# Optimization experiments

Measured on AMD Instinct MI355X. Metric: run time of the kernel, lower is better.

## Reference

```python
import jax, jax.numpy as jnp
import numpy as np

HEADS = 16
LN_EPS = 1e-5

def setup_inputs() -> dict:
    key = jax.random.key(0)
    ks = jax.random.split(key, 8)
    B, S, NT = 4, 1024, 1024
    sc = 1.0 / np.sqrt(NT)
    return {
        "x": jax.random.normal(ks[0], (B, S, NT), dtype=jnp.float32),
        "Wq": jax.random.normal(ks[1], (NT, NT), dtype=jnp.float32) * sc,
        "bq": jax.random.normal(ks[2], (NT,), dtype=jnp.float32) * 0.02,
        "Wk": jax.random.normal(ks[3], (NT, NT), dtype=jnp.float32) * sc,
        "bk": jax.random.normal(ks[4], (NT,), dtype=jnp.float32) * 0.02,
        "Wv": jax.random.normal(ks[5], (NT, NT), dtype=jnp.float32) * sc,
        "bv": jax.random.normal(ks[6], (NT,), dtype=jnp.float32) * 0.02,
        "gamma": jnp.ones((NT,), dtype=jnp.float32),
        "beta": jnp.zeros((NT,), dtype=jnp.float32),
    }

def reference(x, Wq, bq, Wk, bk, Wv, bv, gamma, beta):
    B, S, nt = x.shape
    heads = HEADS
    dph = nt // heads
    # torch nn.Linear: y = x @ W.T + b
    q = x @ Wq.T + bq
    k = x @ Wk.T + bk
    v = x @ Wv.T + bv
    # torch .view(B*heads, -1, dph) is a row-major reshape (interleaved split)
    q = q.reshape(B * heads, -1, dph)
    k = k.reshape(B * heads, -1, dph)
    v = v.reshape(B * heads, -1, dph)
    # scaled scores; scale uses last dim of the score matrix (== seq len here)
    att = jnp.einsum('bid,bjd->bij', q, k)
    scale = att.shape[-1] ** (-0.5)
    att = jax.nn.softmax(jax.nn.relu(att * scale), axis=-1)
    # dropout in eval mode -> identity
    at_sum_sum = att.sum(axis=1).reshape(B, heads, -1)  # [B, heads, S]
    context = jnp.einsum('bij,bjd->bid', att, v).reshape(B, -1, nt)
    h = x + context
    mu = h.mean(axis=-1, keepdims=True)
    var = h.var(axis=-1, keepdims=True)
    out = (h - mu) * jax.lax.rsqrt(var + LN_EPS) * gamma + beta
    return out, at_sum_sum
```

## Files before the change

### kernel.cpp

```cpp
#include <hip/hip_runtime.h>
#include <hip/hip_bf16.h>
#include <cstdint>
#include <cstddef>


typedef short short8 __attribute__((ext_vector_type(8)));
typedef short short4v __attribute__((ext_vector_type(4)));
typedef float f32x4 __attribute__((ext_vector_type(4)));

#define MFMA32(a, b, c) __builtin_amdgcn_mfma_f32_16x16x32_bf16(a, b, c, 0, 0, 0)
#define MFMA16x16(a, b, c) __builtin_amdgcn_mfma_f32_16x16x16bf16_1k(a, b, c, 0, 0, 0)
#define QSCALE 0.045084220027780106f

__device__ __forceinline__ short f2bf(float f) {
  union { float f; uint32_t u; } x; x.f = f;
  uint32_t u = x.u + 0x7fffu + ((x.u >> 16) & 1u);
  return (short)(u >> 16);
}

__device__ __forceinline__ uint32_t pk_bf16_trunc(float lo, float hi) {
  return __builtin_amdgcn_perm(__float_as_uint(hi), __float_as_uint(lo),
                               0x07060302u);
}

#define GLDS16(gp, lp)                                                        \
  __builtin_amdgcn_global_load_lds(                                           \
      (const __attribute__((address_space(1))) void*)(gp),                    \
      (__attribute__((address_space(3))) void*)(lp), 16, 0, 0)

__global__ __launch_bounds__(256) void convert_kernel(
    const float* __restrict__ x, const float* __restrict__ wq,
    const float* __restrict__ wk, const float* __restrict__ wv,
    short* __restrict__ xb, short* __restrict__ wb,
    float* __restrict__ out2) {
  if (blockIdx.x >= 7168) {
    const int idx = (blockIdx.x - 7168) * 256 + threadIdx.x;
    *(f32x4*)(out2 + (size_t)idx * 4) = (f32x4){0.f, 0.f, 0.f, 0.f};
    return;
  }
  const long XN = 4L * 1024 * 1024, WN = 1024L * 1024;
  long e = (long)(blockIdx.x * blockDim.x + threadIdx.x) * 4;
  const float* src; short* dst;
  if (e < XN)               { src = x  + e;                dst = xb + e; }
  else if (e < XN + WN)     { src = wq + (e - XN);         dst = wb + (e - XN); }
  else if (e < XN + 2 * WN) { src = wk + (e - XN - WN);    dst = wb + (e - XN); }
  else                      { src = wv + (e - XN - 2*WN);  dst = wb + (e - XN); }
  f32x4 v = *(const f32x4*)src;
  short4v o;
  o[0] = f2bf(v[0]); o[1] = f2bf(v[1]); o[2] = f2bf(v[2]); o[3] = f2bf(v[3]);
  *(short4v*)dst = o;
}

__global__ __launch_bounds__(256, 3) void qkv_gemm(
    const short* __restrict__ xb, const short* __restrict__ wb,
    const float* __restrict__ bq, const float* __restrict__ bk,
    const float* __restrict__ bv, short* __restrict__ qb,
    short* __restrict__ kb, short* __restrict__ vtp) {
  __shared__ short As[128 * 64];
  __shared__ short Bs[128 * 64];
  const int tid = threadIdx.x;
  const int lane = tid & 63;
  const int lm = lane & 15, quad = lane >> 4;
  const int wave = tid >> 6, wy = wave >> 1, wx = wave & 1;
  const int f = blockIdx.x + (blockIdx.y << 3);
  const int r8 = f & 7, s = f >> 3;
  const int m0 = (((r8 >> 1) << 3) + (s & 7)) * 128;
  const int n0 = (((r8 & 1) << 2) + (s >> 3)) * 128;
  const int z = blockIdx.z;
  const short* w = wb + (size_t)z * (1024 * 1024);
  const float* bias = (z == 0) ? bq : (z == 1) ? bk : bv;
  const float scl = (z == 0) ? QSCALE : 1.0f;

  const int srow = tid >> 3;
  const int schk = (tid & 7) ^ (srow & 7);
  const short* gA = xb + (size_t)(m0 + srow) * 1024 + schk * 8;
  const short* gB = w  + (size_t)(n0 + srow) * 1024 + schk * 8;
  short* lA = As + tid * 8;
  short* lB = Bs + tid * 8;

  f32x4 acc[4][4];
#pragma unroll
  for (int i = 0; i < 4; i++)
#pragma unroll
    for (int j = 0; j < 4; j++) acc[i][j] = (f32x4){0.f, 0.f, 0.f, 0.f};

  for (int k0 = 0; k0 < 1024; k0 += 64) {
#pragma unroll
    for (int q = 0; q < 4; q++) {
      GLDS16(gA + k0 + q * 32 * 1024, lA + q * 2048);
      GLDS16(gB + k0 + q * 32 * 1024, lB + q * 2048);
    }
    __syncthreads();
#pragma unroll
    for (int ks = 0; ks < 2; ks++) {
      const int ck = (((ks << 2) + quad) ^ (lm & 7)) * 8;
      short8 a[4], b[4];
#pragma unroll
      for (int t = 0; t < 4; t++) {
        a[t] = *(const short8*)(As + (wy * 64 + t * 16 + lm) * 64 + ck);
        b[t] = *(const short8*)(Bs + (wx * 64 + t * 16 + lm) * 64 + ck);
      }
#pragma unroll
      for (int mt = 0; mt < 4; mt++)
#pragma unroll
        for (int nt = 0; nt < 4; nt++)
          acc[mt][nt] = MFMA32(a[mt], b[nt], acc[mt][nt]);
    }
    __syncthreads();
  }
  if (z == 2) {
#pragma unroll
    for (int nt = 0; nt < 4; nt++) {
      const int n = n0 + wx * 64 + nt * 16 + lm;
      const float bn = bias[n];
      const size_t nbase = (size_t)((n >> 4) & 3) * 16384 +
                           (size_t)((((n >> 8) & 3) * 16 + (n & 15)) * 4 +
                                    ((n >> 6) & 3));
#pragma unroll
      for (int mt = 0; mt < 4; mt++) {
#pragma unroll
        for (int r = 0; r < 4; r++) {
          const int m = m0 + wy * 64 + mt * 16 + quad * 4 + r;
          vtp[(size_t)(m >> 6) * 65536 + nbase + (size_t)(m & 63) * 256] =
              f2bf(acc[mt][nt][r] + bn);
        }
      }
    }
  } else {
    short* out = (z == 0) ? qb : kb;
#pragma unroll
    for (int nt = 0; nt < 4; nt++) {
      const int n = n0 + wx * 64 + nt * 16 + lm;
      const float bn = bias[n];
#pragma unroll
      for (int mt = 0; mt < 4; mt++) {
        const int mb = m0 + wy * 64 + mt * 16 + quad * 4;
#pragma unroll
        for (int r = 0; r < 4; r++)
          out[(size_t)(mb + r) * 1024 + n] = f2bf((acc[mt][nt][r] + bn) * scl);
      }
    }
  }
}

__global__ __launch_bounds__(256, 2) void attn_kernel(
    const short* __restrict__ qb, const short* __restrict__ kb,
    const short* __restrict__ vtp, const float* __restrict__ x,
    const float* __restrict__ gamma, const float* __restrict__ beta,
    float* __restrict__ out1, float* __restrict__ rvW) {
  __shared__ short Ks[3][64 * 64];

  const int tid = threadIdx.x;
  const int lane = tid & 63, wave = tid >> 6;
  const int lm = lane & 15, quad = lane >> 4;
  const int bid = blockIdx.x;
  const int h = ((bid >> 6) << 3) + (bid & 7);
  const int bb = (bid >> 3) & 7;
  const short* Qh = qb + (size_t)h * 65536;
  const short* Kh = kb + (size_t)h * 65536;
  const short* Vp = vtp + (size_t)h * 65536;
  const int i0 = bb * 128 + wave * 32;

  const short8 qA0 = *(const short8*)(Qh + (size_t)(i0 + lm) * 64 + quad * 8);
  const short8 qA1 = *(const short8*)(Qh + (size_t)(i0 + lm) * 64 + 32 + quad * 8);
  const short8 qB0 = *(const short8*)(Qh + (size_t)(i0 + 16 + lm) * 64 + quad * 8);
  const short8 qB1 = *(const short8*)(Qh + (size_t)(i0 + 16 + lm) * 64 + 32 + quad * 8);

  const int c0 = tid, c1 = tid + 256;
  const short* gK0 = Kh + (size_t)(c0 >> 3) * 64 + ((c0 & 7) ^ ((c0 >> 3) & 7)) * 8;
  const short* gK1 = Kh + (size_t)(c1 >> 3) * 64 + ((c1 & 7) ^ ((c1 >> 3) & 7)) * 8;
  const int lK0 = c0 * 8, lK1 = c1 * 8;
  const short* vl = Vp + lane * 4;

#define ATTN_STAGE(c, buf)                                                    \
  do {                                                                        \
    const int ko_ = ((c) & 15) * 4096;                                        \
    GLDS16(gK0 + ko_, &Ks[buf][0] + lK0);                                     \
    GLDS16(gK1 + ko_, &Ks[buf][0] + lK1);                                     \
  } while (0)

  f32x4 accA[4], accB[4];
#pragma unroll
  for (int t = 0; t < 4; t++) {
    accA[t] = (f32x4){0.f, 0.f, 0.f, 0.f};
    accB[t] = (f32x4){0.f, 0.f, 0.f, 0.f};
  }
  float dsA[4] = {0.f, 0.f, 0.f, 0.f};
  float dsB[4] = {0.f, 0.f, 0.f, 0.f};

  const int swz0 = (quad ^ (lm & 7)) * 8;
  const int swz1 = ((quad + 4) ^ (lm & 7)) * 8;

  ATTN_STAGE(0, 0);
  ATTN_STAGE(1, 1);

  for (int ch = 0; ch < 16; ch++) {
    const int b = ch % 3, bs = (ch + 2) % 3;
    asm volatile("s_waitcnt vmcnt(2)" ::: "memory");
    __builtin_amdgcn_s_barrier();
    __builtin_amdgcn_s_setprio(1);
    const short* vc = vl + ch * 1024;
#pragma unroll
    for (int jj = 0; jj < 4; jj++) {
      const short* krow = &Ks[b][(jj * 16 + lm) * 64];
      const short8 kf0 = *(const short8*)(krow + swz0);
      const short8 kf1 = *(const short8*)(krow + swz1);
      f32x4 zA = {0.f, 0.f, 0.f, 0.f};
      zA = MFMA32(kf0, qA0, zA);
      zA = MFMA32(kf1, qA1, zA);
      f32x4 zB = {0.f, 0.f, 0.f, 0.f};
      zB = MFMA32(kf0, qB0, zB);
      zB = MFMA32(kf1, qB1, zB);
      float pA[4], pB[4];
#pragma unroll
      for (int r = 0; r < 4; r++) {
        pA[r] = __builtin_amdgcn_exp2f(fmaxf(zA[r], 0.f));
        dsA[r] += pA[r];
        pB[r] = __builtin_amdgcn_exp2f(fmaxf(zB[r], 0.f));
        dsB[r] += pB[r];
      }
      union { uint32_t u[2]; short4v s; } puA, puB;
      puA.u[0] = pk_bf16_trunc(pA[0], pA[1]);
      puA.u[1] = pk_bf16_trunc(pA[2], pA[3]);
      puB.u[0] = pk_bf16_trunc(pB[0], pB[1]);
      puB.u[1] = pk_bf16_trunc(pB[2], pB[3]);
      const short* vj = vc + jj * 256;
#pragma unroll
      for (int dt = 0; dt < 4; dt++) {
        const short4v vtf = *(const short4v*)(vj + dt * 16384);
        accA[dt] = MFMA16x16(vtf, puA.s, accA[dt]);
        accB[dt] = MFMA16x16(vtf, puB.s, accB[dt]);
      }
    }
    __builtin_amdgcn_s_setprio(0);
    if (ch < 15) ATTN_STAGE(ch + 2, bs);
  }
  asm volatile("s_waitcnt vmcnt(0)" ::: "memory");

  float tA = (dsA[0] + dsA[1]) + (dsA[2] + dsA[3]);
  tA += __shfl_xor(tA, 16);
  tA += __shfl_xor(tA, 32);
  float tB = (dsB[0] + dsB[1]) + (dsB[2] + dsB[3]);
  tB += __shfl_xor(tB, 16);
  tB += __shfl_xor(tB, 32);
  const float rvA = 1.f / tA;
  const float rvB = 1.f / tB;
  if (lane < 16) {
    rvW[h * 1024 + i0 + lm] = rvA;
    rvW[h * 1024 + i0 + 16 + lm] = rvB;
  }

  const int mA = h * 64 + bb * 8 + wave * 2;
  const int nb = lm * 64 + quad * 4;
#pragma unroll
  for (int tile = 0; tile < 2; tile++) {
    const int m = mA + tile;
    const f32x4* accT = tile ? accB : accA;
    const float rv = tile ? rvB : rvA;
    const float* xr = x + (size_t)m * 1024;
    float hv[4][4], s1 = 0.f, s2 = 0.f;
#pragma unroll
    for (int dt = 0; dt < 4; dt++) {
      f32x4 xv = *(const f32x4*)(xr + nb + dt * 16);
#pragma unroll
      for (int r = 0; r < 4; r++) {
        const float v = xv[r] + accT[dt][r] * rv;
        hv[dt][r] = v; s1 += v; s2 += v * v;
      }
    }
#pragma unroll
    for (int mk = 1; mk < 64; mk <<= 1) {
      s1 += __shfl_xor(s1, mk);
      s2 += __shfl_xor(s2, mk);
    }
    const float mu = s1 * (1.f / 1024.f);
    const float var = s2 * (1.f / 1024.f) - mu * mu;
    const float rstd = rsqrtf(var + 1e-5f);
    float* orow = out1 + (size_t)m * 1024;
#pragma unroll
    for (int dt = 0; dt < 4; dt++) {
      f32x4 gv = *(const f32x4*)(gamma + nb + dt * 16);
      f32x4 bv2 = *(const f32x4*)(beta + nb + dt * 16);
      f32x4 ov;
#pragma unroll
      for (int r = 0; r < 4; r++)
        ov[r] = (hv[dt][r] - mu) * rstd * gv[r] + bv2[r];
      *(f32x4*)(orow + nb + dt * 16) = ov;
    }
  }
}

__global__ __launch_bounds__(256, 4) void colsum_kernel(
    const short* __restrict__ qb, const short* __restrict__ kb,
    const float* __restrict__ rvW, float* __restrict__ out2) {
  const int tid = threadIdx.x;
  const int lane = tid & 63, wave = tid >> 6;
  const int lm = lane & 15, quad = lane >> 4;
  const int bid = blockIdx.x;
  const int h = ((bid >> 7) << 3) + (bid & 7);
  const int jb = (bid >> 3) & 7;
  const int ih = (bid >> 6) & 1;
  const int j0 = jb * 128 + wave * 32;
  const short* Qh = qb + (size_t)h * 65536 + (size_t)ih * 32768;
  const short* Kh = kb + (size_t)h * 65536;
  const float* rvh = rvW + h * 1024 + ih * 512;

  const short* krA = Kh + (size_t)(j0 + lm) * 64 + quad * 8;
  const short8 kA0 = *(const short8*)krA;
  const short8 kA1 = *(const short8*)(krA + 32);
  const short* krB = Kh + (size_t)(j0 + 16 + lm) * 64 + quad * 8;
  const short8 kB0 = *(const short8*)krB;
  const short8 kB1 = *(const short8*)(krB + 32);

  f32x4 csA = {0.f, 0.f, 0.f, 0.f};
  f32x4 csB = {0.f, 0.f, 0.f, 0.f};

  for (int ch = 0; ch < 8; ch++) {
    const short* qc = Qh + ch * 4096 + (size_t)lm * 64 + quad * 8;
    const float* rvc = rvh + ch * 64 + lm;
    __builtin_amdgcn_s_setprio(1);
#pragma unroll
    for (int ii = 0; ii < 4; ii++) {
      const short* qrow = qc + ii * 1024;
      const short8 qf0 = *(const short8*)qrow;
      const short8 qf1 = *(const short8*)(qrow + 32);
      f32x4 zA = {0.f, 0.f, 0.f, 0.f};
      zA = MFMA32(kA0, qf0, zA);
      zA = MFMA32(kA1, qf1, zA);
      f32x4 zB = {0.f, 0.f, 0.f, 0.f};
      zB = MFMA32(kB0, qf0, zB);
      zB = MFMA32(kB1, qf1, zB);
      const float rvv = rvc[ii * 16];
#pragma unroll
      for (int r = 0; r < 4; r++) {
        csA[r] += __builtin_amdgcn_exp2f(fmaxf(zA[r], 0.f)) * rvv;
        csB[r] += __builtin_amdgcn_exp2f(fmaxf(zB[r], 0.f)) * rvv;
      }
    }
    __builtin_amdgcn_s_setprio(0);
  }

#pragma unroll
  for (int mk = 1; mk < 16; mk <<= 1)
#pragma unroll
    for (int r = 0; r < 4; r++) {
      csA[r] += __shfl_xor(csA[r], mk);
      csB[r] += __shfl_xor(csB[r], mk);
    }
  if (lm == 0) {
    float* pA = out2 + h * 1024 + j0 + quad * 4;
    float* pB = pA + 16;
#pragma unroll
    for (int r = 0; r < 4; r++) {
      atomicAdd(pA + r, csA[r]);
      atomicAdd(pB + r, csB[r]);
    }
  }
}

extern "C" void kernel_launch(void* const* d_in, const int* in_sizes, int n_in,
                              void* d_out, int out_size, void* d_ws, size_t ws_size,
                              hipStream_t stream) {
  const float* x  = (const float*)d_in[0];
  const float* Wq = (const float*)d_in[1];
  const float* bq = (const float*)d_in[2];
  const float* Wk = (const float*)d_in[3];
  const float* bk = (const float*)d_in[4];
  const float* Wv = (const float*)d_in[5];
  const float* bv = (const float*)d_in[6];
  const float* gamma = (const float*)d_in[7];
  const float* beta  = (const float*)d_in[8];

  float* out1 = (float*)d_out;
  float* out2 = out1 + 4L * 1024 * 1024;

  short* xb = (short*)d_ws;
  short* wb = xb + 4L * 1024 * 1024;
  short* qb = wb + 3L * 1024 * 1024;
  short* kb = qb + 4L * 1024 * 1024;
  short* vtp = kb + 4L * 1024 * 1024;
  float* rvW = (float*)wb;

  convert_kernel<<<7232, 256, 0, stream>>>(x, Wq, Wk, Wv, xb, wb, out2);
  qkv_gemm<<<dim3(8, 32, 3), 256, 0, stream>>>(xb, wb, bq, bk, bv, qb, kb, vtp);
  attn_kernel<<<512, 256, 0, stream>>>(qb, kb, vtp, x, gamma, beta, out1, rvW);
  colsum_kernel<<<1024, 256, 0, stream>>>(qb, kb, rvW, out2);
}
```

Measured before the change: 181.3 us.

## Fuse column-sum pass into attention kernel and stage V through LDS

Removes the separate colsum kernel. After the softmax denominators are known, the attention block recomputes its 128-row slice of scores against all keys, reduces the normalised probabilities per column in LDS, and issues one atomicAdd per column per block. V tiles are now loaded into a triple-buffered shared buffer alongside K, and the prefetch is issued right after the barrier instead of at the end of the loop. This drops a kernel launch and the rvW round trip through global memory. The cost is a second QK pass inside the attention kernel, extra LDS use that may lower occupancy, and more atomics on out2.

```diff
diff --git a/kernel.cpp b/kernel.cpp
--- a/kernel.cpp
+++ b/kernel.cpp
@@ -147,8 +147,9 @@
     const short* __restrict__ qb, const short* __restrict__ kb,
     const short* __restrict__ vtp, const float* __restrict__ x,
     const float* __restrict__ gamma, const float* __restrict__ beta,
-    float* __restrict__ out1, float* __restrict__ rvW) {
+    float* __restrict__ out1, float* __restrict__ out2) {
   __shared__ short Ks[3][64 * 64];
+  __shared__ short Vs[3][4 * 4 * 256];
 
   const int tid = threadIdx.x;
   const int lane = tid & 63, wave = tid >> 6;
@@ -169,10 +170,20 @@
   const int c0 = tid, c1 = tid + 256;
   const short* gK0 = Kh + (size_t)(c0 >> 3) * 64 + ((c0 & 7) ^ ((c0 >> 3) & 7)) * 8;
   const short* gK1 = Kh + (size_t)(c1 >> 3) * 64 + ((c1 & 7) ^ ((c1 >> 3) & 7)) * 8;
+  const short* gV0 = Vp + (c0 >> 7) * 16384 + ((c0 >> 5) & 3) * 256 + (c0 & 31) * 8;
+  const short* gV1 = Vp + (c1 >> 7) * 16384 + ((c1 >> 5) & 3) * 256 + (c1 & 31) * 8;
   const int lK0 = c0 * 8, lK1 = c1 * 8;
-  const short* vl = Vp + lane * 4;
 
 #define ATTN_STAGE(c, buf)                                                    \
+  do {                                                                        \
+    const int ko_ = ((c) & 15) * 4096, vo_ = ((c) & 15) * 1024;               \
+    GLDS16(gK0 + ko_, &Ks[buf][0] + lK0);                                     \
+    GLDS16(gK1 + ko_, &Ks[buf][0] + lK1);                                     \
+    GLDS16(gV0 + vo_, &Vs[buf][0] + lK0);                                     \
+    GLDS16(gV1 + vo_, &Vs[buf][0] + lK1);                                     \
+  } while (0)
+
+#define ATTN_STAGE2(c, buf)                                                   \
   do {                                                                        \
     const int ko_ = ((c) & 15) * 4096;                                        \
     GLDS16(gK0 + ko_, &Ks[buf][0] + lK0);                                     \
@@ -196,10 +207,10 @@
 
   for (int ch = 0; ch < 16; ch++) {
     const int b = ch % 3, bs = (ch + 2) % 3;
-    asm volatile("s_waitcnt vmcnt(2)" ::: "memory");
+    asm volatile("s_waitcnt vmcnt(4)" ::: "memory");
     __builtin_amdgcn_s_barrier();
+    if (ch < 15) ATTN_STAGE(ch + 2, bs);
     __builtin_amdgcn_s_setprio(1);
-    const short* vc = vl + ch * 1024;
 #pragma unroll
     for (int jj = 0; jj < 4; jj++) {
       const short* krow = &Ks[b][(jj * 16 + lm) * 64];
@@ -224,16 +235,15 @@
       puA.u[1] = pk_bf16_trunc(pA[2], pA[3]);
       puB.u[0] = pk_bf16_trunc(pB[0], pB[1]);
       puB.u[1] = pk_bf16_trunc(pB[2], pB[3]);
-      const short* vj = vc + jj * 256;
+      const short* vbase = &Vs[b][jj * 256 + lane * 4];
 #pragma unroll
       for (int dt = 0; dt < 4; dt++) {
-        const short4v vtf = *(const short4v*)(vj + dt * 16384);
+        const short4v vtf = *(const short4v*)(vbase + dt * 1024);
         accA[dt] = MFMA16x16(vtf, puA.s, accA[dt]);
         accB[dt] = MFMA16x16(vtf, puB.s, accB[dt]);
       }
     }
     __builtin_amdgcn_s_setprio(0);
-    if (ch < 15) ATTN_STAGE(ch + 2, bs);
   }
   asm volatile("s_waitcnt vmcnt(0)" ::: "memory");
 
@@ -245,9 +255,56 @@
   tB += __shfl_xor(tB, 32);
   const float rvA = 1.f / tA;
   const float rvB = 1.f / tB;
-  if (lane < 16) {
-    rvW[h * 1024 + i0 + lm] = rvA;
-    rvW[h * 1024 + i0 + 16 + lm] = rvB;
+
+  float rvsA[4], rvsB[4];
+#pragma unroll
+  for (int r = 0; r < 4; r++) {
+    rvsA[r] = __shfl(rvA, quad * 4 + r);
+    rvsB[r] = __shfl(rvB, quad * 4 + r);
+  }
+  __syncthreads();
+  float* cs = (float*)&Vs[0][0];
+
+  ATTN_STAGE2(0, 0);
+  ATTN_STAGE2(1, 1);
+
+  for (int ch = 0; ch < 16; ch++) {
+    const int b = ch % 3, bs = (ch + 2) % 3;
+    asm volatile("s_waitcnt vmcnt(2)" ::: "memory");
+    __builtin_amdgcn_s_barrier();
+    if (ch < 15) ATTN_STAGE2(ch + 2, bs);
+    __builtin_amdgcn_s_setprio(1);
+#pragma unroll
+    for (int jj = 0; jj < 4; jj++) {
+      const short* krow = &Ks[b][(jj * 16 + lm) * 64];
+      const short8 kf0 = *(const short8*)(krow + swz0);
+      const short8 kf1 = *(const short8*)(krow + swz1);
+      f32x4 zA = {0.f, 0.f, 0.f, 0.f};
+      zA = MFMA32(qA0, kf0, zA);
+      zA = MFMA32(qA1, kf1, zA);
+      f32x4 zB = {0.f, 0.f, 0.f, 0.f};
+      zB = MFMA32(qB0, kf0, zB);
+      zB = MFMA32(qB1, kf1, zB);
+      float v = 0.f;
+#pragma unroll
+      for (int r = 0; r < 4; r++) {
+        v += __builtin_amdgcn_exp2f(fmaxf(zA[r], 0.f)) * rvsA[r]
+           + __builtin_amdgcn_exp2f(fmaxf(zB[r], 0.f)) * rvsB[r];
+      }
+      v += __shfl_xor(v, 16);
+      v += __shfl_xor(v, 32);
+      if (quad == 0)
+        cs[wave * 1024 + ch * 64 + jj * 16 + lm] = v;
+    }
+    __builtin_amdgcn_s_setprio(0);
+  }
+  asm volatile("s_waitcnt vmcnt(0)" ::: "memory");
+  __syncthreads();
+#pragma unroll
+  for (int s = 0; s < 4; s++) {
+    const int j = s * 256 + tid;
+    const float t4 = (cs[j] + cs[1024 + j]) + (cs[2048 + j] + cs[3072 + j]);
+    atomicAdd(out2 + h * 1024 + j, t4);
   }
 
   const int mA = h * 64 + bb * 8 + wave * 2;
@@ -286,74 +343,6 @@
       for (int r = 0; r < 4; r++)
         ov[r] = (hv[dt][r] - mu) * rstd * gv[r] + bv2[r];
       *(f32x4*)(orow + nb + dt * 16) = ov;
-    }
-  }
-}
-
-__global__ __launch_bounds__(256, 4) void colsum_kernel(
-    const short* __restrict__ qb, const short* __restrict__ kb,
-    const float* __restrict__ rvW, float* __restrict__ out2) {
-  const int tid = threadIdx.x;
-  const int lane = tid & 63, wave = tid >> 6;
-  const int lm = lane & 15, quad = lane >> 4;
-  const int bid = blockIdx.x;
-  const int h = ((bid >> 7) << 3) + (bid & 7);
-  const int jb = (bid >> 3) & 7;
-  const int ih = (bid >> 6) & 1;
-  const int j0 = jb * 128 + wave * 32;
-  const short* Qh = qb + (size_t)h * 65536 + (size_t)ih * 32768;
-  const short* Kh = kb + (size_t)h * 65536;
-  const float* rvh = rvW + h * 1024 + ih * 512;
-
-  const short* krA = Kh + (size_t)(j0 + lm) * 64 + quad * 8;
-  const short8 kA0 = *(const short8*)krA;
-  const short8 kA1 = *(const short8*)(krA + 32);
-  const short* krB = Kh + (size_t)(j0 + 16 + lm) * 64 + quad * 8;
-  const short8 kB0 = *(const short8*)krB;
-  const short8 kB1 = *(const short8*)(krB + 32);
-
-  f32x4 csA = {0.f, 0.f, 0.f, 0.f};
-  f32x4 csB = {0.f, 0.f, 0.f, 0.f};
-
-  for (int ch = 0; ch < 8; ch++) {
-    const short* qc = Qh + ch * 4096 + (size_t)lm * 64 + quad * 8;
-    const float* rvc = rvh + ch * 64 + lm;
-    __builtin_amdgcn_s_setprio(1);
-#pragma unroll
-    for (int ii = 0; ii < 4; ii++) {
-      const short* qrow = qc + ii * 1024;
-      const short8 qf0 = *(const short8*)qrow;
-      const short8 qf1 = *(const short8*)(qrow + 32);
-      f32x4 zA = {0.f, 0.f, 0.f, 0.f};
-      zA = MFMA32(kA0, qf0, zA);
-      zA = MFMA32(kA1, qf1, zA);
-      f32x4 zB = {0.f, 0.f, 0.f, 0.f};
-      zB = MFMA32(kB0, qf0, zB);
-      zB = MFMA32(kB1, qf1, zB);
-      const float rvv = rvc[ii * 16];
-#pragma unroll
-      for (int r = 0; r < 4; r++) {
-        csA[r] += __builtin_amdgcn_exp2f(fmaxf(zA[r], 0.f)) * rvv;
-        csB[r] += __builtin_amdgcn_exp2f(fmaxf(zB[r], 0.f)) * rvv;
-      }
-    }
-    __builtin_amdgcn_s_setprio(0);
-  }
-
-#pragma unroll
-  for (int mk = 1; mk < 16; mk <<= 1)
-#pragma unroll
-    for (int r = 0; r < 4; r++) {
-      csA[r] += __shfl_xor(csA[r], mk);
-      csB[r] += __shfl_xor(csB[r], mk);
-    }
-  if (lm == 0) {
-    float* pA = out2 + h * 1024 + j0 + quad * 4;
-    float* pB = pA + 16;
-#pragma unroll
-    for (int r = 0; r < 4; r++) {
-      atomicAdd(pA + r, csA[r]);
-      atomicAdd(pB + r, csB[r]);
     }
   }
 }
@@ -379,10 +368,8 @@
   short* qb = wb + 3L * 1024 * 1024;
   short* kb = qb + 4L * 1024 * 1024;
   short* vtp = kb + 4L * 1024 * 1024;
-  float* rvW = (float*)wb;
 
   convert_kernel<<<7232, 256, 0, stream>>>(x, Wq, Wk, Wv, xb, wb, out2);
   qkv_gemm<<<dim3(8, 32, 3), 256, 0, stream>>>(xb, wb, bq, bk, bv, qb, kb, vtp);
-  attn_kernel<<<512, 256, 0, stream>>>(qb, kb, vtp, x, gamma, beta, out1, rvW);
-  colsum_kernel<<<1024, 256, 0, stream>>>(qb, kb, rvW, out2);
-}
+  attn_kernel<<<512, 256, 0, stream>>>(qb, kb, vtp, x, gamma, beta, out1, out2);
+}
```

Result: faster. 164.4 us (-9.3%).
